# Kernel tuning notes

Hardware: AMD Instinct MI355X
Metric: run time of the kernel (lower is better)

The kernel has to match this reference:

```python
import jax, jax.numpy as jnp
import numpy as np


def setup_inputs() -> dict:
    key = jax.random.key(0)
    kq, kk, kv = jax.random.split(key, 3)
    d_head, sq, skv = 128, 8192, 8192
    q = jax.random.normal(kq, (d_head, sq), dtype=jnp.float32)
    k = jax.random.normal(kk, (d_head, skv), dtype=jnp.float32)
    v = jax.random.normal(kv, (d_head, skv), dtype=jnp.float32)
    return {"q": q, "k": k, "v": v}


def reference(q, k, v):
    # qk: (seqlen_q, seqlen_kv) -- full score matrix, no 1/sqrt(d) scaling (faithful)
    qk = jnp.einsum('dq,dk->qk', q, k)
    row_max = jnp.max(qk, axis=1, keepdims=True)
    exp_row = jnp.exp(qk - row_max)
    scores = exp_row / jnp.sum(exp_row, axis=1, keepdims=True)
    # attn_out: (seqlen_q, d_head)
    attn_out = jnp.einsum('qk,dk->qd', scores, v)
    return attn_out
```

## Files before the change

### kernel.cpp

```cpp
#include <hip/hip_runtime.h>
#include <hip/hip_bf16.h>
#include <math.h>

typedef _Float16 half8 __attribute__((ext_vector_type(8)));
typedef _Float16 half4v __attribute__((ext_vector_type(4)));
typedef __fp16 fp16x2 __attribute__((ext_vector_type(2)));
typedef float f32x4 __attribute__((ext_vector_type(4)));
typedef float f32x16 __attribute__((ext_vector_type(16)));

#define D 128
#define SQ 8192
#define SKV 8192
#define BQ 128
#define BKV 64
#define LOG2E 1.4426950408889634f
#define DEFER_THR 11.5417f

__device__ __forceinline__ ushort f2bf(float x) {
  union { float f; unsigned u; } v; v.f = x;
  unsigned r = v.u + 0x7fffu + ((v.u >> 16) & 1u);
  return (ushort)(r >> 16);
}
__device__ __forceinline__ float bf2f(ushort h) {
  union { unsigned u; float f; } v; v.u = ((unsigned)h) << 16;
  return v.f;
}
__device__ __forceinline__ unsigned cvtpk_bf(float a, float b) {
  unsigned r;
  asm("v_cvt_pk_bf16_f32 %0, %1, %2" : "=v"(r) : "v"(a), "v"(b));
  return r;
}
__device__ __forceinline__ unsigned cvtpk_h(float a, float b) {
  union { fp16x2 h; unsigned u; } r;
  r.h = __builtin_amdgcn_cvt_pkrtz(a, b);
  return r.u;
}
__device__ __forceinline__ float fexp2(float x) {
  float r;
  asm("v_exp_f32 %0, %1" : "=v"(r) : "v"(x));
  return r;
}
__device__ __forceinline__ void pl32swap(unsigned& a, unsigned& b) {
  asm("v_permlane32_swap_b32 %0, %1" : "+v"(a), "+v"(b));
}

__global__ void prep_q(const float* __restrict__ src, _Float16* __restrict__ dst) {
  __shared__ float tile[32][33];
  int s0 = blockIdx.x * 32, d0 = blockIdx.y * 32;
  int t = threadIdx.x, g = t >> 5, l = t & 31;
#pragma unroll
  for (int j = 0; j < 4; ++j)
    tile[g * 4 + j][l] = src[(size_t)(d0 + g * 4 + j) * SQ + s0 + l];
  __syncthreads();
#pragma unroll
  for (int j = 0; j < 4; ++j) {
    int sl = g * 4 + j;
    dst[(size_t)(s0 + sl) * D + d0 + l] = (_Float16)(tile[l][sl] * LOG2E);
  }
}

__global__ void prep_k(const float* __restrict__ src, _Float16* __restrict__ dst) {
  __shared__ float tile[32][33];
  int s0 = blockIdx.x * 32, d0 = blockIdx.y * 32;
  int t = threadIdx.x, g = t >> 5, l = t & 31;
#pragma unroll
  for (int j = 0; j < 4; ++j)
    tile[g * 4 + j][l] = src[(size_t)(d0 + g * 4 + j) * SKV + s0 + l];
  __syncthreads();
#pragma unroll
  for (int j = 0; j < 4; ++j) {
    int srow = s0 + g * 4 + j;
    int dcol = d0 + l;
    size_t elem = (size_t)((srow >> 5) * 8 + (dcol >> 4)) * 512 +
                  (((dcol >> 3) & 1) * 32 + (srow & 31)) * 8 + (dcol & 7);
    dst[elem] = (_Float16)tile[l][g * 4 + j];
  }
}

__global__ void prep_v(const float* __restrict__ src, _Float16* __restrict__ dst) {
  int i4 = (blockIdx.x * 256 + threadIdx.x) * 4;
  float4 v = *(const float4*)(src + i4);
  int drow = i4 >> 13;
  int kv = i4 & (SKV - 1);
  size_t elem = (size_t)(kv >> 6) * 8192 +
                (size_t)((drow >> 5) * 4 + ((kv >> 4) & 3)) * 512 +
                (((kv >> 3) & 1) * 32 + (drow & 31)) * 8 + (kv & 7);
  half4v o = { (_Float16)v.x, (_Float16)v.y, (_Float16)v.z, (_Float16)v.w };
  *(half4v*)(dst + elem) = o;
}

__global__ __launch_bounds__(256, 2)
void flash_fwd(const _Float16* __restrict__ QT, const _Float16* __restrict__ PK,
               const _Float16* __restrict__ PV,
               ushort* __restrict__ Opart, float* __restrict__ Mst,
               float* __restrict__ Lst, int splitLen) {
  __shared__ _Float16 Kl[2][BKV * D];
  __shared__ _Float16 Vl[2][BKV * D];

  const int tid = threadIdx.x;
  const int w = tid >> 6;
  const int lane = tid & 63;
  const int lc = lane & 31;
  const int hi = lane >> 5;
  const int qb = blockIdx.x;
  const int split = blockIdx.y;
  const int qrow = qb * BQ + w * 32 + lc;

  half8 qh[8];
#pragma unroll
  for (int ds = 0; ds < 8; ++ds)
    qh[ds] = *(const half8*)(QT + (size_t)qrow * D + ds * 16 + hi * 8);

  f32x16 Ot[4];
#pragma unroll
  for (int dt = 0; dt < 4; ++dt)
#pragma unroll
    for (int e = 0; e < 16; ++e) Ot[dt][e] = 0.f;
  float mrun = -INFINITY, lrun = 0.f;

  const int kvBase = split * splitLen;
  const int nsteps = splitLen / BKV;

#define STAGE(NB, KV0)                                                        \
  {                                                                           \
    _Pragma("unroll")                                                         \
    for (int j = 0; j < 8; ++j) {                                             \
      int cblk = w * 8 + j;                                                   \
      int cc = cblk & 15;                                                     \
      const _Float16* gp = ((cblk < 16) ? PK : PV) +                          \
                           (size_t)(KV0) * D + cc * 512 + lane * 8;           \
      _Float16* lp = ((cblk < 16) ? &Kl[NB][0] : &Vl[NB][0]) + cc * 512;      \
      __builtin_amdgcn_global_load_lds(                                       \
          (const __attribute__((address_space(1))) unsigned*)gp,              \
          (__attribute__((address_space(3))) unsigned*)lp, 16, 0, 0);         \
    }                                                                         \
  }

  STAGE(0, kvBase);
  __syncthreads();
  int cur = 0;

  for (int it = 0; it < nsteps; ++it) {
    const int kv0 = kvBase + it * BKV;
    const bool more = (it + 1 < nsteps);
    if (more) STAGE(cur ^ 1, kv0 + BKV);

    const _Float16* kb = &Kl[cur][0] + lane * 8;
    const _Float16* vb = &Vl[cur][0] + lane * 8;

    half8 ka[16];
#pragma unroll
    for (int j = 0; j < 16; ++j) ka[j] = *(const half8*)(kb + j * 512);

    f32x16 s0, s1;
#pragma unroll
    for (int e = 0; e < 16; ++e) { s0[e] = 0.f; s1[e] = 0.f; }
    __builtin_amdgcn_s_setprio(1);
#pragma unroll
    for (int ds = 0; ds < 8; ++ds) {
      s0 = __builtin_amdgcn_mfma_f32_32x32x16_f16(ka[ds], qh[ds], s0, 0, 0, 0);
      s1 = __builtin_amdgcn_mfma_f32_32x32x16_f16(ka[8 + ds], qh[ds], s1, 0, 0, 0);
    }
    __builtin_amdgcn_s_setprio(0);

    half8 va[16];
#pragma unroll
    for (int f = 0; f < 16; ++f) va[f] = *(const half8*)(vb + f * 512);

    float t8[8];
#pragma unroll
    for (int e = 0; e < 8; ++e)
      t8[e] = fmaxf(fmaxf(s0[e], s0[e + 8]), fmaxf(s1[e], s1[e + 8]));
    float mx = fmaxf(fmaxf(fmaxf(t8[0], t8[4]), fmaxf(t8[1], t8[5])),
                     fmaxf(fmaxf(t8[2], t8[6]), fmaxf(t8[3], t8[7])));
    mx = fmaxf(mx, __shfl_xor(mx, 32));

    if (!__all(mx - mrun <= DEFER_THR)) {
      float mn = fmaxf(mrun, mx);
      float sc = fexp2(mrun - mn);
      mrun = mn;
      lrun *= sc;
#pragma unroll
      for (int dt = 0; dt < 4; ++dt)
#pragma unroll
        for (int e = 0; e < 16; ++e) Ot[dt][e] *= sc;
    }

#pragma unroll
    for (int e = 0; e < 16; ++e) {
      s0[e] = fexp2(s0[e] - mrun);
      s1[e] = fexp2(s1[e] - mrun);
    }
    float a8[8];
#pragma unroll
    for (int e = 0; e < 8; ++e) a8[e] = (s0[e] + s0[e + 8]) + (s1[e] + s1[e + 8]);
    float lsum = ((a8[0] + a8[4]) + (a8[1] + a8[5])) +
                 ((a8[2] + a8[6]) + (a8[3] + a8[7]));
    lsum += __shfl_xor(lsum, 32);
    lrun += lsum;

    unsigned pk[8];
    half8 pb[4];
    union { unsigned u[4]; half8 v; } pbu;
#pragma unroll
    for (int j = 0; j < 8; ++j) pk[j] = cvtpk_h(s0[2 * j], s0[2 * j + 1]);
    pl32swap(pk[0], pk[2]); pl32swap(pk[1], pk[3]);
    pl32swap(pk[4], pk[6]); pl32swap(pk[5], pk[7]);
    pbu.u[0] = pk[0]; pbu.u[1] = pk[1]; pbu.u[2] = pk[2]; pbu.u[3] = pk[3]; pb[0] = pbu.v;
    pbu.u[0] = pk[4]; pbu.u[1] = pk[5]; pbu.u[2] = pk[6]; pbu.u[3] = pk[7]; pb[1] = pbu.v;
#pragma unroll
    for (int j = 0; j < 8; ++j) pk[j] = cvtpk_h(s1[2 * j], s1[2 * j + 1]);
    pl32swap(pk[0], pk[2]); pl32swap(pk[1], pk[3]);
    pl32swap(pk[4], pk[6]); pl32swap(pk[5], pk[7]);
    pbu.u[0] = pk[0]; pbu.u[1] = pk[1]; pbu.u[2] = pk[2]; pbu.u[3] = pk[3]; pb[2] = pbu.v;
    pbu.u[0] = pk[4]; pbu.u[1] = pk[5]; pbu.u[2] = pk[6]; pbu.u[3] = pk[7]; pb[3] = pbu.v;

    __builtin_amdgcn_s_setprio(1);
#pragma unroll
    for (int cc = 0; cc < 4; ++cc) {
      Ot[0] = __builtin_amdgcn_mfma_f32_32x32x16_f16(va[0 * 4 + cc], pb[cc], Ot[0], 0, 0, 0);
      Ot[1] = __builtin_amdgcn_mfma_f32_32x32x16_f16(va[1 * 4 + cc], pb[cc], Ot[1], 0, 0, 0);
      Ot[2] = __builtin_amdgcn_mfma_f32_32x32x16_f16(va[2 * 4 + cc], pb[cc], Ot[2], 0, 0, 0);
      Ot[3] = __builtin_amdgcn_mfma_f32_32x32x16_f16(va[3 * 4 + cc], pb[cc], Ot[3], 0, 0, 0);
    }
    __builtin_amdgcn_s_setprio(0);

    __syncthreads();
    cur ^= 1;
  }

  ushort* Op = Opart + (size_t)split * SQ * D + (size_t)qrow * D;
#pragma unroll
  for (int dt = 0; dt < 4; ++dt) {
#pragma unroll
    for (int rg = 0; rg < 4; ++rg) {
      uint2 o2;
      o2.x = cvtpk_bf(Ot[dt][4 * rg + 0], Ot[dt][4 * rg + 1]);
      o2.y = cvtpk_bf(Ot[dt][4 * rg + 2], Ot[dt][4 * rg + 3]);
      *(uint2*)(Op + dt * 32 + rg * 8 + hi * 4) = o2;
    }
  }
  if (hi == 0) {
    Mst[split * SQ + qrow] = mrun;
    Lst[split * SQ + qrow] = lrun;
  }
}

__global__ void combine(const ushort* __restrict__ Opart, const float* __restrict__ Mst,
                        const float* __restrict__ Lst, float* __restrict__ out, int nsplit) {
  int t4 = (blockIdx.x * 256 + threadIdx.x) * 4;
  int qi = t4 >> 7;
  float M = -INFINITY;
  for (int s = 0; s < nsplit; ++s) M = fmaxf(M, Mst[s * SQ + qi]);
  float n0 = 0.f, n1 = 0.f, n2 = 0.f, n3 = 0.f, den = 0.f;
  for (int s = 0; s < nsplit; ++s) {
    float wgt = fexp2(Mst[s * SQ + qi] - M);
    den += wgt * Lst[s * SQ + qi];
    ushort4 u = *(const ushort4*)(Opart + (size_t)s * SQ * D + t4);
    n0 += wgt * bf2f(u.x); n1 += wgt * bf2f(u.y);
    n2 += wgt * bf2f(u.z); n3 += wgt * bf2f(u.w);
  }
  float inv = 1.0f / den;
  float4 o = { n0 * inv, n1 * inv, n2 * inv, n3 * inv };
  *(float4*)(out + t4) = o;
}

extern "C" void kernel_launch(void* const* d_in, const int* in_sizes, int n_in,
                              void* d_out, int out_size, void* d_ws, size_t ws_size,
                              hipStream_t stream) {
  const float* q = (const float*)d_in[0];
  const float* k = (const float*)d_in[1];
  const float* v = (const float*)d_in[2];
  float* out = (float*)d_out;

  char* ws = (char*)d_ws;
  const size_t mat = (size_t)SQ * D * 2;
  _Float16* QT = (_Float16*)(ws);
  _Float16* PK = (_Float16*)(ws + mat);
  _Float16* PV = (_Float16*)(ws + 2 * mat);
  char* rest = ws + 3 * mat;

  const size_t opartSz = (size_t)SQ * D * 2;
  const size_t statSz  = (size_t)SQ * 4;
  int nsplit = 8;
  while (nsplit > 1 &&
         3 * mat + (size_t)nsplit * (opartSz + 2 * statSz) > ws_size) nsplit >>= 1;

  ushort* Opart = (ushort*)rest;
  float* Mst = (float*)(rest + (size_t)nsplit * opartSz);
  float* Lst = (float*)(rest + (size_t)nsplit * opartSz + (size_t)nsplit * statSz);

  prep_q<<<dim3(SQ / 32, D / 32), 256, 0, stream>>>(q, QT);
  prep_k<<<dim3(SKV / 32, D / 32), 256, 0, stream>>>(k, PK);
  prep_v<<<(D * SKV) / (256 * 4), 256, 0, stream>>>(v, PV);
  flash_fwd<<<dim3(SQ / BQ, nsplit), 256, 0, stream>>>(QT, PK, PV,
                                                       Opart, Mst, Lst, SKV / nsplit);
  combine<<<(SQ * D) / (256 * 4), 256, 0, stream>>>(Opart, Mst, Lst, out, nsplit);
}
```

Measured before the change: 65.45 us.

## Single-buffer V tile to fit three blocks per CU, use uneven 12-way KV split

V is now loaded into one shared buffer per iteration, issued at the start of the step and read only after a mid-loop barrier, while K stays double-buffered. This cuts LDS per block from 64KB to 48KB so launch bounds can ask for three blocks per CU. The KV range is split 12 ways with uneven tile partitioning, giving more blocks to fill the GPU. In exchange there is an extra barrier per step, the V load latency is less hidden, and registers are tighter under the higher occupancy target.

```diff
diff --git a/kernel.cpp b/kernel.cpp
--- a/kernel.cpp
+++ b/kernel.cpp
@@ -13,6 +13,7 @@
 #define SKV 8192
 #define BQ 128
 #define BKV 64
+#define TILES (SKV / BKV)
 #define LOG2E 1.4426950408889634f
 #define DEFER_THR 11.5417f
 
@@ -89,13 +90,13 @@
   *(half4v*)(dst + elem) = o;
 }
 
-__global__ __launch_bounds__(256, 2)
+__global__ __launch_bounds__(256, 3)
 void flash_fwd(const _Float16* __restrict__ QT, const _Float16* __restrict__ PK,
                const _Float16* __restrict__ PV,
                ushort* __restrict__ Opart, float* __restrict__ Mst,
-               float* __restrict__ Lst, int splitLen) {
+               float* __restrict__ Lst, int nsplit) {
   __shared__ _Float16 Kl[2][BKV * D];
-  __shared__ _Float16 Vl[2][BKV * D];
+  __shared__ _Float16 Vl[BKV * D];
 
   const int tid = threadIdx.x;
   const int w = tid >> 6;
@@ -106,6 +107,10 @@
   const int split = blockIdx.y;
   const int qrow = qb * BQ + w * 32 + lc;
 
+  const int t0 = (split * TILES) / nsplit;
+  const int t1 = ((split + 1) * TILES) / nsplit;
+  const int nT = t1 - t0;
+
   half8 qh[8];
 #pragma unroll
   for (int ds = 0; ds < 8; ++ds)
@@ -118,35 +123,41 @@
     for (int e = 0; e < 16; ++e) Ot[dt][e] = 0.f;
   float mrun = -INFINITY, lrun = 0.f;
 
-  const int kvBase = split * splitLen;
-  const int nsteps = splitLen / BKV;
-
-#define STAGE(NB, KV0)                                                        \
+#define STAGE_K(NB, T)                                                        \
   {                                                                           \
     _Pragma("unroll")                                                         \
-    for (int j = 0; j < 8; ++j) {                                             \
-      int cblk = w * 8 + j;                                                   \
-      int cc = cblk & 15;                                                     \
-      const _Float16* gp = ((cblk < 16) ? PK : PV) +                          \
-                           (size_t)(KV0) * D + cc * 512 + lane * 8;           \
-      _Float16* lp = ((cblk < 16) ? &Kl[NB][0] : &Vl[NB][0]) + cc * 512;      \
+    for (int j = 0; j < 4; ++j) {                                             \
+      int cc = w * 4 + j;                                                     \
+      const _Float16* gp = PK + (size_t)(T) * (BKV * D) + cc * 512 + lane * 8;\
+      _Float16* lp = &Kl[NB][0] + cc * 512;                                   \
       __builtin_amdgcn_global_load_lds(                                       \
           (const __attribute__((address_space(1))) unsigned*)gp,              \
           (__attribute__((address_space(3))) unsigned*)lp, 16, 0, 0);         \
     }                                                                         \
   }
-
-  STAGE(0, kvBase);
+#define STAGE_V(T)                                                            \
+  {                                                                           \
+    _Pragma("unroll")                                                         \
+    for (int j = 0; j < 4; ++j) {                                             \
+      int cc = w * 4 + j;                                                     \
+      const _Float16* gp = PV + (size_t)(T) * (BKV * D) + cc * 512 + lane * 8;\
+      _Float16* lp = &Vl[0] + cc * 512;                                       \
+      __builtin_amdgcn_global_load_lds(                                       \
+          (const __attribute__((address_space(1))) unsigned*)gp,              \
+          (__attribute__((address_space(3))) unsigned*)lp, 16, 0, 0);         \
+    }                                                                         \
+  }
+
+  STAGE_K(0, t0);
   __syncthreads();
   int cur = 0;
 
-  for (int it = 0; it < nsteps; ++it) {
-    const int kv0 = kvBase + it * BKV;
-    const bool more = (it + 1 < nsteps);
-    if (more) STAGE(cur ^ 1, kv0 + BKV);
+  for (int it = 0; it < nT; ++it) {
+    const int t = t0 + it;
+    STAGE_V(t);
+    if (it + 1 < nT) STAGE_K(cur ^ 1, t + 1);
 
     const _Float16* kb = &Kl[cur][0] + lane * 8;
-    const _Float16* vb = &Vl[cur][0] + lane * 8;
 
     half8 ka[16];
 #pragma unroll
@@ -162,10 +173,6 @@
       s1 = __builtin_amdgcn_mfma_f32_32x32x16_f16(ka[8 + ds], qh[ds], s1, 0, 0, 0);
     }
     __builtin_amdgcn_s_setprio(0);
-
-    half8 va[16];
-#pragma unroll
-    for (int f = 0; f < 16; ++f) va[f] = *(const half8*)(vb + f * 512);
 
     float t8[8];
 #pragma unroll
@@ -199,6 +206,8 @@
     lsum += __shfl_xor(lsum, 32);
     lrun += lsum;
 
+    __syncthreads();
+
     unsigned pk[8];
     half8 pb[4];
     union { unsigned u[4]; half8 v; } pbu;
@@ -214,6 +223,11 @@
     pl32swap(pk[4], pk[6]); pl32swap(pk[5], pk[7]);
     pbu.u[0] = pk[0]; pbu.u[1] = pk[1]; pbu.u[2] = pk[2]; pbu.u[3] = pk[3]; pb[2] = pbu.v;
     pbu.u[0] = pk[4]; pbu.u[1] = pk[5]; pbu.u[2] = pk[6]; pbu.u[3] = pk[7]; pb[3] = pbu.v;
+
+    const _Float16* vb = &Vl[0] + lane * 8;
+    half8 va[16];
+#pragma unroll
+    for (int f = 0; f < 16; ++f) va[f] = *(const half8*)(vb + f * 512);
 
     __builtin_amdgcn_s_setprio(1);
 #pragma unroll
@@ -282,7 +296,7 @@
 
   const size_t opartSz = (size_t)SQ * D * 2;
   const size_t statSz  = (size_t)SQ * 4;
-  int nsplit = 8;
+  int nsplit = 12;
   while (nsplit > 1 &&
          3 * mat + (size_t)nsplit * (opartSz + 2 * statSz) > ws_size) nsplit >>= 1;
 
@@ -294,6 +308,6 @@
   prep_k<<<dim3(SKV / 32, D / 32), 256, 0, stream>>>(k, PK);
   prep_v<<<(D * SKV) / (256 * 4), 256, 0, stream>>>(v, PV);
   flash_fwd<<<dim3(SQ / BQ, nsplit), 256, 0, stream>>>(QT, PK, PV,
-                                                       Opart, Mst, Lst, SKV / nsplit);
+                                                       Opart, Mst, Lst, nsplit);
   combine<<<(SQ * D) / (256 * 4), 256, 0, stream>>>(Opart, Mst, Lst, out, nsplit);
 }
```

Result: slower. 89.79 us (+37.2%).

## Halve KV tile to 32, raise occupancy to 4 blocks, split KV 16 ways

Applied to the files above, without the earlier changes.

Shrinks the KV tile from 64 to 32 and re-lays out the packed K and V buffers to match, which halves the LDS footprint and per-wave register arrays. Launch bounds rise to 4 blocks per CU and the KV split count goes from 8 to 16 to fill more CUs. The aim is better latency hiding through occupancy. In exchange there are twice as many loop iterations, each with a barrier and a softmax reduction, and the combine pass has more partials to merge.

```diff
diff --git a/kernel.cpp b/kernel.cpp
--- a/kernel.cpp
+++ b/kernel.cpp
@@ -12,7 +12,7 @@
 #define SQ 8192
 #define SKV 8192
 #define BQ 128
-#define BKV 64
+#define BKV 32
 #define LOG2E 1.4426950408889634f
 #define DEFER_THR 11.5417f
 
@@ -71,7 +71,7 @@
   for (int j = 0; j < 4; ++j) {
     int srow = s0 + g * 4 + j;
     int dcol = d0 + l;
-    size_t elem = (size_t)((srow >> 5) * 8 + (dcol >> 4)) * 512 +
+    size_t elem = (size_t)(srow >> 5) * 4096 + (size_t)(dcol >> 4) * 512 +
                   (((dcol >> 3) & 1) * 32 + (srow & 31)) * 8 + (dcol & 7);
     dst[elem] = (_Float16)tile[l][g * 4 + j];
   }
@@ -82,14 +82,14 @@
   float4 v = *(const float4*)(src + i4);
   int drow = i4 >> 13;
   int kv = i4 & (SKV - 1);
-  size_t elem = (size_t)(kv >> 6) * 8192 +
-                (size_t)((drow >> 5) * 4 + ((kv >> 4) & 3)) * 512 +
+  size_t elem = (size_t)(kv >> 5) * 4096 +
+                (size_t)((drow >> 5) * 2 + ((kv >> 4) & 1)) * 512 +
                 (((kv >> 3) & 1) * 32 + (drow & 31)) * 8 + (kv & 7);
   half4v o = { (_Float16)v.x, (_Float16)v.y, (_Float16)v.z, (_Float16)v.w };
   *(half4v*)(dst + elem) = o;
 }
 
-__global__ __launch_bounds__(256, 2)
+__global__ __launch_bounds__(256, 4)
 void flash_fwd(const _Float16* __restrict__ QT, const _Float16* __restrict__ PK,
                const _Float16* __restrict__ PV,
                ushort* __restrict__ Opart, float* __restrict__ Mst,
@@ -120,59 +120,56 @@
 
   const int kvBase = split * splitLen;
   const int nsteps = splitLen / BKV;
-
-#define STAGE(NB, KV0)                                                        \
+  const int tBase = kvBase / BKV;
+
+#define STAGE(NB, T)                                                          \
   {                                                                           \
     _Pragma("unroll")                                                         \
-    for (int j = 0; j < 8; ++j) {                                             \
-      int cblk = w * 8 + j;                                                   \
-      int cc = cblk & 15;                                                     \
-      const _Float16* gp = ((cblk < 16) ? PK : PV) +                          \
-                           (size_t)(KV0) * D + cc * 512 + lane * 8;           \
-      _Float16* lp = ((cblk < 16) ? &Kl[NB][0] : &Vl[NB][0]) + cc * 512;      \
+    for (int j = 0; j < 4; ++j) {                                             \
+      int cc = w * 4 + j;                                                     \
+      int c8 = cc & 7;                                                        \
+      const _Float16* gp = ((cc < 8) ? PK : PV) +                             \
+                           (size_t)(T) * (BKV * D) + c8 * 512 + lane * 8;     \
+      _Float16* lp = ((cc < 8) ? &Kl[NB][0] : &Vl[NB][0]) + c8 * 512;         \
       __builtin_amdgcn_global_load_lds(                                       \
           (const __attribute__((address_space(1))) unsigned*)gp,              \
           (__attribute__((address_space(3))) unsigned*)lp, 16, 0, 0);         \
     }                                                                         \
   }
 
-  STAGE(0, kvBase);
+  STAGE(0, tBase);
   __syncthreads();
   int cur = 0;
 
   for (int it = 0; it < nsteps; ++it) {
-    const int kv0 = kvBase + it * BKV;
     const bool more = (it + 1 < nsteps);
-    if (more) STAGE(cur ^ 1, kv0 + BKV);
+    if (more) STAGE(cur ^ 1, tBase + it + 1);
 
     const _Float16* kb = &Kl[cur][0] + lane * 8;
     const _Float16* vb = &Vl[cur][0] + lane * 8;
 
-    half8 ka[16];
-#pragma unroll
-    for (int j = 0; j < 16; ++j) ka[j] = *(const half8*)(kb + j * 512);
-
-    f32x16 s0, s1;
-#pragma unroll
-    for (int e = 0; e < 16; ++e) { s0[e] = 0.f; s1[e] = 0.f; }
+    half8 ka[8];
+#pragma unroll
+    for (int j = 0; j < 8; ++j) ka[j] = *(const half8*)(kb + j * 512);
+
+    f32x16 s0;
+#pragma unroll
+    for (int e = 0; e < 16; ++e) s0[e] = 0.f;
     __builtin_amdgcn_s_setprio(1);
 #pragma unroll
-    for (int ds = 0; ds < 8; ++ds) {
+    for (int ds = 0; ds < 8; ++ds)
       s0 = __builtin_amdgcn_mfma_f32_32x32x16_f16(ka[ds], qh[ds], s0, 0, 0, 0);
-      s1 = __builtin_amdgcn_mfma_f32_32x32x16_f16(ka[8 + ds], qh[ds], s1, 0, 0, 0);
-    }
     __builtin_amdgcn_s_setprio(0);
 
-    half8 va[16];
-#pragma unroll
-    for (int f = 0; f < 16; ++f) va[f] = *(const half8*)(vb + f * 512);
-
-    float t8[8];
-#pragma unroll
-    for (int e = 0; e < 8; ++e)
-      t8[e] = fmaxf(fmaxf(s0[e], s0[e + 8]), fmaxf(s1[e], s1[e + 8]));
-    float mx = fmaxf(fmaxf(fmaxf(t8[0], t8[4]), fmaxf(t8[1], t8[5])),
-                     fmaxf(fmaxf(t8[2], t8[6]), fmaxf(t8[3], t8[7])));
+    half8 va[8];
+#pragma unroll
+    for (int f = 0; f < 8; ++f) va[f] = *(const half8*)(vb + f * 512);
+
+    float t4a = fmaxf(fmaxf(s0[0], s0[4]), fmaxf(s0[8], s0[12]));
+    float t4b = fmaxf(fmaxf(s0[1], s0[5]), fmaxf(s0[9], s0[13]));
+    float t4c = fmaxf(fmaxf(s0[2], s0[6]), fmaxf(s0[10], s0[14]));
+    float t4d = fmaxf(fmaxf(s0[3], s0[7]), fmaxf(s0[11], s0[15]));
+    float mx = fmaxf(fmaxf(t4a, t4b), fmaxf(t4c, t4d));
     mx = fmaxf(mx, __shfl_xor(mx, 32));
 
     if (!__all(mx - mrun <= DEFER_THR)) {
@@ -187,20 +184,17 @@
     }
 
 #pragma unroll
-    for (int e = 0; e < 16; ++e) {
-      s0[e] = fexp2(s0[e] - mrun);
-      s1[e] = fexp2(s1[e] - mrun);
-    }
-    float a8[8];
-#pragma unroll
-    for (int e = 0; e < 8; ++e) a8[e] = (s0[e] + s0[e + 8]) + (s1[e] + s1[e + 8]);
-    float lsum = ((a8[0] + a8[4]) + (a8[1] + a8[5])) +
-                 ((a8[2] + a8[6]) + (a8[3] + a8[7]));
+    for (int e = 0; e < 16; ++e) s0[e] = fexp2(s0[e] - mrun);
+    float a4a = (s0[0] + s0[4]) + (s0[8] + s0[12]);
+    float a4b = (s0[1] + s0[5]) + (s0[9] + s0[13]);
+    float a4c = (s0[2] + s0[6]) + (s0[10] + s0[14]);
+    float a4d = (s0[3] + s0[7]) + (s0[11] + s0[15]);
+    float lsum = (a4a + a4b) + (a4c + a4d);
     lsum += __shfl_xor(lsum, 32);
     lrun += lsum;
 
     unsigned pk[8];
-    half8 pb[4];
+    half8 pb[2];
     union { unsigned u[4]; half8 v; } pbu;
 #pragma unroll
     for (int j = 0; j < 8; ++j) pk[j] = cvtpk_h(s0[2 * j], s0[2 * j + 1]);
@@ -208,20 +202,12 @@
     pl32swap(pk[4], pk[6]); pl32swap(pk[5], pk[7]);
     pbu.u[0] = pk[0]; pbu.u[1] = pk[1]; pbu.u[2] = pk[2]; pbu.u[3] = pk[3]; pb[0] = pbu.v;
     pbu.u[0] = pk[4]; pbu.u[1] = pk[5]; pbu.u[2] = pk[6]; pbu.u[3] = pk[7]; pb[1] = pbu.v;
-#pragma unroll
-    for (int j = 0; j < 8; ++j) pk[j] = cvtpk_h(s1[2 * j], s1[2 * j + 1]);
-    pl32swap(pk[0], pk[2]); pl32swap(pk[1], pk[3]);
-    pl32swap(pk[4], pk[6]); pl32swap(pk[5], pk[7]);
-    pbu.u[0] = pk[0]; pbu.u[1] = pk[1]; pbu.u[2] = pk[2]; pbu.u[3] = pk[3]; pb[2] = pbu.v;
-    pbu.u[0] = pk[4]; pbu.u[1] = pk[5]; pbu.u[2] = pk[6]; pbu.u[3] = pk[7]; pb[3] = pbu.v;
 
     __builtin_amdgcn_s_setprio(1);
 #pragma unroll
-    for (int cc = 0; cc < 4; ++cc) {
-      Ot[0] = __builtin_amdgcn_mfma_f32_32x32x16_f16(va[0 * 4 + cc], pb[cc], Ot[0], 0, 0, 0);
-      Ot[1] = __builtin_amdgcn_mfma_f32_32x32x16_f16(va[1 * 4 + cc], pb[cc], Ot[1], 0, 0, 0);
-      Ot[2] = __builtin_amdgcn_mfma_f32_32x32x16_f16(va[2 * 4 + cc], pb[cc], Ot[2], 0, 0, 0);
-      Ot[3] = __builtin_amdgcn_mfma_f32_32x32x16_f16(va[3 * 4 + cc], pb[cc], Ot[3], 0, 0, 0);
+    for (int dt = 0; dt < 4; ++dt) {
+      Ot[dt] = __builtin_amdgcn_mfma_f32_32x32x16_f16(va[dt * 2 + 0], pb[0], Ot[dt], 0, 0, 0);
+      Ot[dt] = __builtin_amdgcn_mfma_f32_32x32x16_f16(va[dt * 2 + 1], pb[1], Ot[dt], 0, 0, 0);
     }
     __builtin_amdgcn_s_setprio(0);
 
@@ -282,7 +268,7 @@
 
   const size_t opartSz = (size_t)SQ * D * 2;
   const size_t statSz  = (size_t)SQ * 4;
-  int nsplit = 8;
+  int nsplit = 16;
   while (nsplit > 1 &&
          3 * mat + (size_t)nsplit * (opartSz + 2 * statSz) > ws_size) nsplit >>= 1;
 
```

Measured after the change: 114.4 us. 74.8% more time.
